# Kernel tuning notes

Hardware: AMD Instinct MI355X
Metric: run time of the kernel (lower is better)

## Reference

```python
import jax, jax.numpy as jnp
import numpy as np

LOG2 = float(np.log(2.0))

def ssp(v):
    # shifted softplus used by SchNet-style nets
    return jax.nn.softplus(v) - LOG2

N = 100000   # nodes per set
E = 600000   # edges
A = 128      # n_atom_basis
F = 128      # n_filters
R = 20       # n_rbf


def setup_inputs() -> dict:
    key = jax.random.key(0)
    ks = jax.random.split(key, 20)
    def lin(k, fan_in, fan_out):
        return jax.random.normal(k, (fan_in, fan_out), dtype=jnp.float32) / np.sqrt(fan_in)
    inp = {
        "x": jax.random.normal(ks[0], (N, A), dtype=jnp.float32),
        "y": jax.random.normal(ks[1], (N, A), dtype=jnp.float32),
        "f_ij": jax.random.uniform(ks[2], (E, R), dtype=jnp.float32),
        "rcut_ij": jax.random.uniform(ks[3], (E,), dtype=jnp.float32),
        "idx_i": jax.random.randint(ks[4], (E,), 0, N),
        "idx_j": jax.random.randint(ks[5], (E,), 0, N),
        # in2f / in2f_y: Dense(A, F, bias=False)
        "W_in2f": lin(ks[6], A, F),
        "W_in2f_y": lin(ks[7], A, F),
        # filter_network: Dense(R, F, act) -> Dense(F, F)
        "Wf1": lin(ks[8], R, F), "bf1": jnp.zeros((F,), jnp.float32),
        "Wf2": lin(ks[9], F, F), "bf2": jnp.zeros((F,), jnp.float32),
        # f2out: Dense(F, A, act) -> Dense(A, A)
        "Wx1": lin(ks[10], F, A), "bx1": jnp.zeros((A,), jnp.float32),
        "Wx2": lin(ks[11], A, A), "bx2": jnp.zeros((A,), jnp.float32),
        # f2out_y
        "Wy1": lin(ks[12], F, A), "by1": jnp.zeros((A,), jnp.float32),
        "Wy2": lin(ks[13], A, A), "by2": jnp.zeros((A,), jnp.float32),
    }
    return inp


def reference(x, y, f_ij, rcut_ij, W_in2f, W_in2f_y, Wf1, bf1, Wf2, bf2,
              Wx1, bx1, Wx2, bx2, Wy1, by1, Wy2, by2, idx_i, idx_j):
    # node feature projections (bias-free)
    xf = x @ W_in2f                # [N, F]
    yf = y @ W_in2f_y              # [N, F]
    # edge filter MLP
    Wij = ssp(f_ij @ Wf1 + bf1) @ Wf2 + bf2      # [E, F]
    Wij = Wij * rcut_ij[:, None]
    # gather-multiply
    x_ij = yf[idx_j] * Wij          # messages into x-nodes
    y_ij = xf[idx_i] * Wij          # messages into y-nodes
    # scatter_add into dual node sets
    conv_x = jax.ops.segment_sum(x_ij, idx_i, num_segments=N)   # [N, F]
    conv_y = jax.ops.segment_sum(y_ij, idx_j, num_segments=N)   # [N, F]
    # output MLPs
    out_x = ssp(conv_x @ Wx1 + bx1) @ Wx2 + bx2
    out_y = ssp(conv_y @ Wy1 + by1) @ Wy2 + by2
    return (out_x, out_y)
```

## Files before the change

kernel.cpp:

```cpp
#include <hip/hip_runtime.h>
#include <hip/hip_bf16.h>

#define NF 128
#define RBF 20

using short8 = __attribute__((ext_vector_type(8))) short;
using half8  = __attribute__((ext_vector_type(8))) _Float16;
using f32x4  = __attribute__((ext_vector_type(4))) float;

__device__ __forceinline__ float sspf(float v) {
    const float t = __expf(-fabsf(v));
    return fmaxf(v, 0.f) + __logf(1.f + t) - 0.69314718055994531f;
}
__device__ __forceinline__ unsigned short f2bf(float f) {
    union { float f; unsigned u; } v; v.f = f;
    unsigned r = v.u + 0x7fffu + ((v.u >> 16) & 1u);
    return (unsigned short)(r >> 16);
}
__device__ __forceinline__ float bf2f(unsigned short s) {
    union { unsigned u; float f; } v; v.u = ((unsigned)s) << 16;
    return v.f;
}

__global__ void hist1_kernel(const int* __restrict__ idx, int* __restrict__ deg, int E)
{
    for (int e = blockIdx.x * blockDim.x + threadIdx.x; e < E;
         e += gridDim.x * blockDim.x)
        atomicAdd(&deg[idx[e]], 1);
}

__global__ void scanA1_kernel(const int* __restrict__ deg, int* __restrict__ loc,
                              int* __restrict__ parts, int NN)
{
    const int tid = threadIdx.x;
    const int base = blockIdx.x * 2048;
    __shared__ int tsum[256];
    int v[8]; int s = 0;
    #pragma unroll
    for (int r = 0; r < 8; ++r) {
        const int idx = base + tid * 8 + r;
        v[r] = (idx < NN) ? deg[idx] : 0;
        s += v[r];
    }
    tsum[tid] = s;
    __syncthreads();
    #pragma unroll
    for (int d = 1; d < 256; d <<= 1) {
        const int add = (tid >= d) ? tsum[tid - d] : 0;
        __syncthreads();
        tsum[tid] += add;
        __syncthreads();
    }
    int run = tsum[tid] - s;
    #pragma unroll
    for (int r = 0; r < 8; ++r) {
        const int idx = base + tid * 8 + r;
        if (idx < NN) loc[idx] = run;
        run += v[r];
    }
    if (tid == 0) parts[blockIdx.x] = tsum[255];
}

__global__ void scanB1_kernel(int* __restrict__ parts, int NB)
{
    __shared__ int p[64];
    const int t = threadIdx.x;
    p[t] = (t < NB) ? parts[t] : 0;
    __syncthreads();
    #pragma unroll
    for (int d = 1; d < 64; d <<= 1) {
        const int add = (t >= d) ? p[t - d] : 0;
        __syncthreads();
        p[t] += add;
        __syncthreads();
    }
    parts[t] = (t > 0) ? p[t - 1] : 0;
}

__global__ void scanC1_kernel(const int* __restrict__ loc, const int* __restrict__ parts,
                              int* __restrict__ rowp, int* __restrict__ cur, int NN)
{
    for (int i = blockIdx.x * blockDim.x + threadIdx.x; i < NN;
         i += gridDim.x * blockDim.x) {
        const int v = loc[i] + parts[i >> 11];
        rowp[i] = v;
        cur[i]  = v;
    }
}

__global__ void scatter1_kernel(const int* __restrict__ idx_i, const int* __restrict__ idx_j,
                                const float* __restrict__ rcut,
                                int* __restrict__ cur, int* __restrict__ ord,
                                int* __restrict__ nis, int* __restrict__ jos,
                                float* __restrict__ rcs, int E)
{
    for (int e = blockIdx.x * blockDim.x + threadIdx.x; e < E;
         e += gridDim.x * blockDim.x) {
        const int key = idx_i[e];
        const int p = atomicAdd(&cur[key], 1);
        ord[p] = e;
        nis[p] = key;
        jos[p] = idx_j[e] * NF;
        rcs[p] = rcut[e];
    }
}

__global__ void fsort_kernel(const float* __restrict__ f_ij,
                             const int* __restrict__ ord,
                             _Float16* __restrict__ f16s, int E)
{
    for (int p = blockIdx.x * blockDim.x + threadIdx.x; p < E;
         p += gridDim.x * blockDim.x) {
        const int e = ord[p];
        const float* src = f_ij + (size_t)e * RBF;
        _Float16* dst = f16s + (size_t)p * 32;
        #pragma unroll
        for (int k4 = 0; k4 < 5; ++k4) {
            const float4 v = *reinterpret_cast<const float4*>(src + k4 * 4);
            dst[k4 * 4 + 0] = (_Float16)v.x;
            dst[k4 * 4 + 1] = (_Float16)v.y;
            dst[k4 * 4 + 2] = (_Float16)v.z;
            dst[k4 * 4 + 3] = (_Float16)v.w;
        }
        #pragma unroll
        for (int k = RBF; k < 32; ++k) dst[k] = (_Float16)0.f;
    }
}

__global__ __launch_bounds__(256, 2)
void edge_hybrid_kernel(const _Float16* __restrict__ f16s,
                        const int* __restrict__ nis,
                        const int* __restrict__ jos,
                        const float* __restrict__ rcs,
                        const float* __restrict__ Wf1,
                        const float* __restrict__ bf1,
                        const float* __restrict__ Wf2,
                        const float* __restrict__ bf2v,
                        const _Float16* __restrict__ xf,
                        const _Float16* __restrict__ yf,
                        const int* __restrict__ rowp,
                        float* __restrict__ conv_x,
                        float* __restrict__ conv_y,
                        int NN, int E)
{
    const int tid = threadIdx.x;
    const int l = tid & 63, w = tid >> 6;
    const int lr = l & 15, lk = l >> 4;
    const int wcol0 = w * 32;

    __shared__ _Float16 M_s[32 * 137];
    __shared__ _Float16 Ash[32 * 136];
    __shared__ _Float16 xown[16 * 136];
    __shared__ int ni_s[32];
    __shared__ int jo_s[32];
    __shared__ float rc_s[32];

    _Float16* fst = M_s;

    half8 b1fr[2];
    #pragma unroll
    for (int cb = 0; cb < 2; ++cb) {
        const int col = wcol0 + cb * 16 + lr;
        #pragma unroll
        for (int j = 0; j < 8; ++j) {
            const int k = lk * 8 + j;
            b1fr[cb][j] = (k < RBF) ? (_Float16)Wf1[k * NF + col] : (_Float16)0.f;
        }
    }
    half8 b2fr[4][2];
    #pragma unroll
    for (int kb = 0; kb < 4; ++kb)
        #pragma unroll
        for (int cb = 0; cb < 2; ++cb) {
            const int col = wcol0 + cb * 16 + lr;
            #pragma unroll
            for (int j = 0; j < 8; ++j)
                b2fr[kb][cb][j] = (_Float16)Wf2[(size_t)(kb * 32 + lk * 8 + j) * NF + col];
        }
    const float b1c[2] = { bf1[wcol0 + lr], bf1[wcol0 + 16 + lr] };
    const float b2c[2] = { bf2v[wcol0 + lr], bf2v[wcol0 + 16 + lr] };

    const int n0 = blockIdx.x * 16;
    const int eb = rowp[n0];
    const int ee = (n0 + 16 < NN) ? rowp[n0 + 16] : E;
    const int nt = (ee - eb + 31) >> 5;

    #pragma unroll
    for (int u = 0; u < 4; ++u) {
        const int tt = u * 256 + tid;
        const int row = tt >> 6, cp = tt & 63;
        unsigned v = 0;
        if (n0 + row < NN)
            v = reinterpret_cast<const unsigned*>(xf)[(size_t)(n0 + row) * 64 + cp];
        *reinterpret_cast<unsigned*>(&xown[row * 136 + cp * 2]) = v;
    }

    f32x4 accS[2] = {};

    for (int t = 0; t < nt; ++t) {
        const int p0 = eb + t * 32;
        const int cnt = ee - p0;
        __syncthreads();

        if (tid < 32) {
            const int p = p0 + tid;
            const bool val = p < ee;
            ni_s[tid] = val ? nis[p] : -1;
            jo_s[tid] = val ? jos[p] : 0;
            rc_s[tid] = val ? rcs[p] : 0.f;
        }
        {
            const unsigned* src = reinterpret_cast<const unsigned*>(f16s);
            unsigned* dst = reinterpret_cast<unsigned*>(fst);
            #pragma unroll
            for (int s2 = 0; s2 < 2; ++s2) {
                const int tt = s2 * 256 + tid;
                int p = p0 + (tt >> 4);
                if (p >= E) p = E - 1;
                dst[tt] = src[(size_t)p * 16 + (tt & 15)];
            }
        }
        __syncthreads();

        f32x4 acc1[2][2] = {};
        #pragma unroll
        for (int rb = 0; rb < 2; ++rb) {
            const half8 a = *reinterpret_cast<const half8*>(
                &fst[(rb * 16 + lr) * 32 + lk * 8]);
            #pragma unroll
            for (int cb = 0; cb < 2; ++cb)
                acc1[rb][cb] = __builtin_amdgcn_mfma_f32_16x16x32_f16(
                    a, b1fr[cb], acc1[rb][cb], 0, 0, 0);
        }
        #pragma unroll
        for (int rb = 0; rb < 2; ++rb)
            #pragma unroll
            for (int cb = 0; cb < 2; ++cb) {
                const int col = wcol0 + cb * 16 + lr;
                #pragma unroll
                for (int q = 0; q < 4; ++q) {
                    const int e = rb * 16 + lk * 4 + q;
                    const float hv = sspf(acc1[rb][cb][q] + b1c[cb]);
                    Ash[e * 136 + (col ^ ((e & 7) << 3))] = (_Float16)hv;
                }
            }
        __syncthreads();

        unsigned gr[8];
        #pragma unroll
        for (int u = 0; u < 8; ++u) {
            const int tt = u * 256 + tid;
            const int slot = tt >> 6, cp = tt & 63;
            gr[u] = reinterpret_cast<const unsigned*>(yf)[(jo_s[slot] >> 1) + cp];
        }

        f32x4 acc2[2][2] = {};
        #pragma unroll
        for (int rb = 0; rb < 2; ++rb) {
            half8 a[4];
            #pragma unroll
            for (int kb = 0; kb < 4; ++kb) {
                const int e  = rb * 16 + lr;
                const int k0 = kb * 32 + lk * 8;
                a[kb] = *reinterpret_cast<const half8*>(
                    &Ash[e * 136 + (k0 ^ ((e & 7) << 3))]);
            }
            #pragma unroll
            for (int cb = 0; cb < 2; ++cb)
                #pragma unroll
                for (int kb = 0; kb < 4; ++kb)
                    acc2[rb][cb] = __builtin_amdgcn_mfma_f32_16x16x32_f16(
                        a[kb], b2fr[kb][cb], acc2[rb][cb], 0, 0, 0);
        }
        __syncthreads();

        #pragma unroll
        for (int u = 0; u < 8; ++u) {
            const int tt = u * 256 + tid;
            const int slot = tt >> 6, cp = tt & 63;
            *reinterpret_cast<unsigned*>(&Ash[slot * 136 + cp * 2]) = gr[u];
        }
        __syncthreads();

        #pragma unroll
        for (int rb = 0; rb < 2; ++rb)
            #pragma unroll
            for (int cb = 0; cb < 2; ++cb) {
                const int col = wcol0 + cb * 16 + lr;
                #pragma unroll
                for (int q = 0; q < 4; ++q) {
                    const int e = rb * 16 + lk * 4 + q;
                    const float wv = (acc2[rb][cb][q] + b2c[cb]) * rc_s[e];
                    const float g  = (float)Ash[e * 136 + col];
                    M_s[e * 137 + col] = (_Float16)(wv * g);
                    if (e < cnt) {
                        const int oi = ni_s[e] - n0;
                        const float xo = (float)xown[oi * 136 + col];
                        unsafeAtomicAdd(&conv_y[(size_t)jo_s[e] + col], xo * wv);
                    }
                }
            }
        __syncthreads();

        {
            half8 as;
            int nn[8];
            #pragma unroll
            for (int j = 0; j < 8; ++j) nn[j] = ni_s[lk * 8 + j];
            const int node = n0 + lr;
            #pragma unroll
            for (int j = 0; j < 8; ++j)
                as[j] = (nn[j] == node) ? (_Float16)1.f : (_Float16)0.f;
            #pragma unroll
            for (int cb = 0; cb < 2; ++cb) {
                const int col = wcol0 + cb * 16 + lr;
                half8 bm;
                #pragma unroll
                for (int j = 0; j < 8; ++j)
                    bm[j] = M_s[(lk * 8 + j) * 137 + col];
                accS[cb] = __builtin_amdgcn_mfma_f32_16x16x32_f16(
                    as, bm, accS[cb], 0, 0, 0);
            }
        }
    }

    #pragma unroll
    for (int cb = 0; cb < 2; ++cb) {
        const int col = wcol0 + cb * 16 + lr;
        #pragma unroll
        for (int q = 0; q < 4; ++q) {
            const int n = n0 + lk * 4 + q;
            if (n < NN) conv_x[(size_t)n * NF + col] = accS[cb][q];
        }
    }
}

__global__ __launch_bounds__(256, 2)
void proj_mfma_kernel(const float* in0, const float* in1,
                      const float* __restrict__ W0, const float* __restrict__ W1p,
                      _Float16* o0, _Float16* o1,
                      float* __restrict__ conv_y, int N)
{
    const float* in = blockIdx.y ? in1 : in0;
    const float* W  = blockIdx.y ? W1p : W0;
    _Float16* out   = blockIdx.y ? o1 : o0;

    const int tid = threadIdx.x;
    const int l = tid & 63, w = tid >> 6;
    const int lr = l & 15, lk = l >> 4;
    const int wcol0 = w * 32;

    __shared__ _Float16 Ahi[64 * NF];

    half8 bfr[4][2];
    #pragma unroll
    for (int kb = 0; kb < 4; ++kb)
        #pragma unroll
        for (int cb = 0; cb < 2; ++cb) {
            const int col = wcol0 + cb * 16 + lr;
            #pragma unroll
            for (int j = 0; j < 8; ++j)
                bfr[kb][cb][j] = (_Float16)W[(size_t)(kb * 32 + lk * 8 + j) * NF + col];
        }

    const int n0 = blockIdx.x * 64;
    #pragma unroll
    for (int s = 0; s < 32; ++s) {
        const int t = s * 256 + tid;
        const int row = t >> 7, cc = t & (NF - 1);
        const float v = (n0 + row < N) ? in[(size_t)(n0 + row) * NF + cc] : 0.f;
        Ahi[row * NF + (cc ^ ((row & 7) << 3))] = (_Float16)v;
    }
    {
        const float4 z = {0.f, 0.f, 0.f, 0.f};
        const int rbase = n0 + 32 * blockIdx.y;
        #pragma unroll
        for (int s = 0; s < 4; ++s) {
            const int t = s * 256 + tid;
            const int row = rbase + (t >> 5);
            if (row < N)
                *reinterpret_cast<float4*>(&conv_y[(size_t)row * NF + (t & 31) * 4]) = z;
        }
    }
    __syncthreads();

    f32x4 acc[4][2] = {};
    #pragma unroll
    for (int rb = 0; rb < 4; ++rb) {
        half8 a[4];
        #pragma unroll
        for (int kb = 0; kb < 4; ++kb) {
            const int e  = rb * 16 + lr;
            const int k0 = kb * 32 + lk * 8;
            a[kb] = *reinterpret_cast<const half8*>(&Ahi[e * NF + (k0 ^ ((e & 7) << 3))]);
        }
        #pragma unroll
        for (int cb = 0; cb < 2; ++cb)
            #pragma unroll
            for (int kb = 0; kb < 4; ++kb)
                acc[rb][cb] = __builtin_amdgcn_mfma_f32_16x16x32_f16(
                    a[kb], bfr[kb][cb], acc[rb][cb], 0, 0, 0);
    }

    #pragma unroll
    for (int rb = 0; rb < 4; ++rb)
        #pragma unroll
        for (int cb = 0; cb < 2; ++cb) {
            const int col = wcol0 + cb * 16 + lr;
            #pragma unroll
            for (int q = 0; q < 4; ++q) {
                const int n = n0 + rb * 16 + lk * 4 + q;
                if (n < N) out[(size_t)n * NF + col] = (_Float16)acc[rb][cb][q];
            }
        }
}

__global__ __launch_bounds__(256, 2)
void out_fused_kernel(const float* conv0, const float* conv1,
                      const float* __restrict__ W10, const float* __restrict__ W11,
                      const float* __restrict__ b10, const float* __restrict__ b11,
                      const float* __restrict__ W20, const float* __restrict__ W21,
                      const float* __restrict__ b20, const float* __restrict__ b21,
                      float* o0, float* o1, int N)
{
    const float* in = blockIdx.y ? conv1 : conv0;
    const float* W1 = blockIdx.y ? W11 : W10;
    const float* b1 = blockIdx.y ? b11 : b10;
    const float* W2 = blockIdx.y ? W21 : W20;
    const float* b2 = blockIdx.y ? b21 : b20;
    float* out      = blockIdx.y ? o1  : o0;

    const int tid = threadIdx.x;
    const int l = tid & 63, w = tid >> 6;
    const int lr = l & 15, lk = l >> 4;
    const int wcol0 = w * 32;

    __shared__ unsigned short Ahi[64 * NF];
    __shared__ unsigned short Alo[64 * NF];

    short8 w1fr[4][2], w2fr[4][2];
    #pragma unroll
    for (int kb = 0; kb < 4; ++kb)
        #pragma unroll
        for (int cb = 0; cb < 2; ++cb) {
            const int col = wcol0 + cb * 16 + lr;
            #pragma unroll
            for (int j = 0; j < 8; ++j) {
                const size_t kk = (size_t)(kb * 32 + lk * 8 + j) * NF + col;
                w1fr[kb][cb][j] = (short)f2bf(W1[kk]);
                w2fr[kb][cb][j] = (short)f2bf(W2[kk]);
            }
        }
    const float b1c0 = b1[wcol0 + lr], b1c1 = b1[wcol0 + 16 + lr];
    const float b2c0 = b2[wcol0 + lr], b2c1 = b2[wcol0 + 16 + lr];

    const int n0 = blockIdx.x * 64;
    #pragma unroll
    for (int s = 0; s < 32; ++s) {
        const int t = s * 256 + tid;
        const int row = t >> 7, cc = t & (NF - 1);
        const float v = (n0 + row < N) ? in[(size_t)(n0 + row) * NF + cc] : 0.f;
        const unsigned short hi = f2bf(v);
        const int idx = row * NF + (cc ^ ((row & 7) << 3));
        Ahi[idx] = hi;
        Alo[idx] = f2bf(v - bf2f(hi));
    }
    __syncthreads();

    f32x4 acc1[4][2] = {};
    #pragma unroll
    for (int rb = 0; rb < 4; ++rb) {
        short8 ah[4], al[4];
        #pragma unroll
        for (int kb = 0; kb < 4; ++kb) {
            const int e  = rb * 16 + lr;
            const int k0 = kb * 32 + lk * 8;
            const int idx = e * NF + (k0 ^ ((e & 7) << 3));
            ah[kb] = *reinterpret_cast<const short8*>(&Ahi[idx]);
            al[kb] = *reinterpret_cast<const short8*>(&Alo[idx]);
        }
        #pragma unroll
        for (int cb = 0; cb < 2; ++cb)
            #pragma unroll
            for (int kb = 0; kb < 4; ++kb) {
                acc1[rb][cb] = __builtin_amdgcn_mfma_f32_16x16x32_bf16(
                    ah[kb], w1fr[kb][cb], acc1[rb][cb], 0, 0, 0);
                acc1[rb][cb] = __builtin_amdgcn_mfma_f32_16x16x32_bf16(
                    al[kb], w1fr[kb][cb], acc1[rb][cb], 0, 0, 0);
            }
    }
    __syncthreads();

    #pragma unroll
    for (int rb = 0; rb < 4; ++rb)
        #pragma unroll
        for (int cb = 0; cb < 2; ++cb) {
            const int col = wcol0 + cb * 16 + lr;
            #pragma unroll
            for (int q = 0; q < 4; ++q) {
                const int e = rb * 16 + lk * 4 + q;
                const float hv = sspf(acc1[rb][cb][q] + (cb ? b1c1 : b1c0));
                const unsigned short hi = f2bf(hv);
                const int idx = e * NF + (col ^ ((e & 7) << 3));
                Ahi[idx] = hi;
                Alo[idx] = f2bf(hv - bf2f(hi));
            }
        }
    __syncthreads();

    f32x4 acc2[4][2] = {};
    #pragma unroll
    for (int rb = 0; rb < 4; ++rb) {
        short8 ah[4], al[4];
        #pragma unroll
        for (int kb = 0; kb < 4; ++kb) {
            const int e  = rb * 16 + lr;
            const int k0 = kb * 32 + lk * 8;
            const int idx = e * NF + (k0 ^ ((e & 7) << 3));
            ah[kb] = *reinterpret_cast<const short8*>(&Ahi[idx]);
            al[kb] = *reinterpret_cast<const short8*>(&Alo[idx]);
        }
        #pragma unroll
        for (int cb = 0; cb < 2; ++cb)
            #pragma unroll
            for (int kb = 0; kb < 4; ++kb) {
                acc2[rb][cb] = __builtin_amdgcn_mfma_f32_16x16x32_bf16(
                    ah[kb], w2fr[kb][cb], acc2[rb][cb], 0, 0, 0);
                acc2[rb][cb] = __builtin_amdgcn_mfma_f32_16x16x32_bf16(
                    al[kb], w2fr[kb][cb], acc2[rb][cb], 0, 0, 0);
            }
    }

    #pragma unroll
    for (int rb = 0; rb < 4; ++rb)
        #pragma unroll
        for (int cb = 0; cb < 2; ++cb) {
            const int col = wcol0 + cb * 16 + lr;
            #pragma unroll
            for (int q = 0; q < 4; ++q) {
                const int n = n0 + rb * 16 + lk * 4 + q;
                if (n < N)
                    out[(size_t)n * NF + col] = acc2[rb][cb][q] + (cb ? b2c1 : b2c0);
            }
        }
}

extern "C" void kernel_launch(void* const* d_in, const int* in_sizes, int n_in,
                              void* d_out, int out_size, void* d_ws, size_t ws_size,
                              hipStream_t stream)
{
    const float* x    = (const float*)d_in[0];
    const float* y    = (const float*)d_in[1];
    const float* f_ij = (const float*)d_in[2];
    const float* rcut = (const float*)d_in[3];
    const int* idx_i  = (const int*)d_in[4];
    const int* idx_j  = (const int*)d_in[5];
    const float* W_in2f   = (const float*)d_in[6];
    const float* W_in2f_y = (const float*)d_in[7];
    const float* Wf1 = (const float*)d_in[8];
    const float* bf1 = (const float*)d_in[9];
    const float* Wf2 = (const float*)d_in[10];
    const float* bf2 = (const float*)d_in[11];
    const float* Wx1 = (const float*)d_in[12];
    const float* bx1 = (const float*)d_in[13];
    const float* Wx2 = (const float*)d_in[14];
    const float* bx2 = (const float*)d_in[15];
    const float* Wy1 = (const float*)d_in[16];
    const float* by1 = (const float*)d_in[17];
    const float* Wy2 = (const float*)d_in[18];
    const float* by2 = (const float*)d_in[19];

    const int N = in_sizes[0] / NF;
    const int E = in_sizes[4];
    const size_t NNF = (size_t)N * NF;

    _Float16* xf = (_Float16*)d_out;
    _Float16* yf = xf + NNF;
    float* ox = (float*)d_out;
    float* oy = ox + NNF;

    char* ub = (char*)d_out + 4 * NNF;
    int* deg   = (int*)ub;
    int* loc   = deg + N;
    int* rowp  = loc + N;
    int* cur   = rowp + N;
    int* parts = cur + N;
    int* ord   = parts + 64;
    int* nis   = ord + E;
    int* jos   = nis + E;
    float* rcs = (float*)(jos + E);
    _Float16* f16s = (_Float16*)(rcs + E);

    float* conv_x = (float*)d_ws;
    float* conv_y = conv_x + NNF;

    const int NB = (N + 2047) / 2048;
    const int nodeTiles = (N + 63) / 64;
    const int nGroups = (N + 15) / 16;

    hipMemsetAsync(deg, 0, (size_t)N * sizeof(int), stream);

    proj_mfma_kernel<<<dim3(nodeTiles, 2), 256, 0, stream>>>(
        x, y, W_in2f, W_in2f_y, xf, yf, conv_y, N);

    hist1_kernel<<<1024, 256, 0, stream>>>(idx_i, deg, E);
    scanA1_kernel<<<NB, 256, 0, stream>>>(deg, loc, parts, N);
    scanB1_kernel<<<1, 64, 0, stream>>>(parts, NB);
    scanC1_kernel<<<128, 256, 0, stream>>>(loc, parts, rowp, cur, N);
    scatter1_kernel<<<1024, 256, 0, stream>>>(idx_i, idx_j, rcut, cur, ord,
                                              nis, jos, rcs, E);
    fsort_kernel<<<2048, 256, 0, stream>>>(f_ij, ord, f16s, E);

    edge_hybrid_kernel<<<nGroups, 256, 0, stream>>>(
        f16s, nis, jos, rcs, Wf1, bf1, Wf2, bf2, xf, yf,
        rowp, conv_x, conv_y, N, E);

    out_fused_kernel<<<dim3(nodeTiles, 2), 256, 0, stream>>>(
        conv_x, conv_y, Wx1, Wy1, bx1, by1, Wx2, Wy2, bx2, by2,
        ox, oy, N);
}
```

Measured before the change: 647.6 us.

## Fuse f_ij sort into scatter, load edge features directly, use single fp16 MFMA in output MLP

Three changes at once. The f_ij conversion and reorder now happen inside the scatter kernel, which removes the ord array and a separate fsort launch, and writes each row with 16-byte stores. The edge kernel reads its f16 A-fragments straight from global memory instead of staging them in LDS, which drops one barrier per tile. The output MLP kernel replaces the split bf16 hi/lo pair of MFMAs with one fp16 MFMA per step, halving that matrix work and its LDS traffic at the cost of precision.

New measurement: 632.5 us. 2.3% less time.

```diff
diff --git a/kernel.cpp b/kernel.cpp
--- a/kernel.cpp
+++ b/kernel.cpp
@@ -4,22 +4,12 @@
 #define NF 128
 #define RBF 20
 
-using short8 = __attribute__((ext_vector_type(8))) short;
-using half8  = __attribute__((ext_vector_type(8))) _Float16;
-using f32x4  = __attribute__((ext_vector_type(4))) float;
+using half8 = __attribute__((ext_vector_type(8))) _Float16;
+using f32x4 = __attribute__((ext_vector_type(4))) float;
 
 __device__ __forceinline__ float sspf(float v) {
     const float t = __expf(-fabsf(v));
     return fmaxf(v, 0.f) + __logf(1.f + t) - 0.69314718055994531f;
-}
-__device__ __forceinline__ unsigned short f2bf(float f) {
-    union { float f; unsigned u; } v; v.f = f;
-    unsigned r = v.u + 0x7fffu + ((v.u >> 16) & 1u);
-    return (unsigned short)(r >> 16);
-}
-__device__ __forceinline__ float bf2f(unsigned short s) {
-    union { unsigned u; float f; } v; v.u = ((unsigned)s) << 16;
-    return v.f;
 }
 
 __global__ void hist1_kernel(const int* __restrict__ idx, int* __restrict__ deg, int E)
@@ -90,40 +80,35 @@
 
 __global__ void scatter1_kernel(const int* __restrict__ idx_i, const int* __restrict__ idx_j,
                                 const float* __restrict__ rcut,
-                                int* __restrict__ cur, int* __restrict__ ord,
+                                const float* __restrict__ f_ij,
+                                int* __restrict__ cur,
                                 int* __restrict__ nis, int* __restrict__ jos,
-                                float* __restrict__ rcs, int E)
+                                float* __restrict__ rcs,
+                                _Float16* __restrict__ f16s, int E)
 {
     for (int e = blockIdx.x * blockDim.x + threadIdx.x; e < E;
          e += gridDim.x * blockDim.x) {
         const int key = idx_i[e];
         const int p = atomicAdd(&cur[key], 1);
-        ord[p] = e;
         nis[p] = key;
         jos[p] = idx_j[e] * NF;
         rcs[p] = rcut[e];
-    }
-}
-
-__global__ void fsort_kernel(const float* __restrict__ f_ij,
-                             const int* __restrict__ ord,
-                             _Float16* __restrict__ f16s, int E)
-{
-    for (int p = blockIdx.x * blockDim.x + threadIdx.x; p < E;
-         p += gridDim.x * blockDim.x) {
-        const int e = ord[p];
+
         const float* src = f_ij + (size_t)e * RBF;
-        _Float16* dst = f16s + (size_t)p * 32;
+        _Float16 tmp[32];
         #pragma unroll
         for (int k4 = 0; k4 < 5; ++k4) {
             const float4 v = *reinterpret_cast<const float4*>(src + k4 * 4);
-            dst[k4 * 4 + 0] = (_Float16)v.x;
-            dst[k4 * 4 + 1] = (_Float16)v.y;
-            dst[k4 * 4 + 2] = (_Float16)v.z;
-            dst[k4 * 4 + 3] = (_Float16)v.w;
-        }
-        #pragma unroll
-        for (int k = RBF; k < 32; ++k) dst[k] = (_Float16)0.f;
+            tmp[k4 * 4 + 0] = (_Float16)v.x;
+            tmp[k4 * 4 + 1] = (_Float16)v.y;
+            tmp[k4 * 4 + 2] = (_Float16)v.z;
+            tmp[k4 * 4 + 3] = (_Float16)v.w;
+        }
+        #pragma unroll
+        for (int k = RBF; k < 32; ++k) tmp[k] = (_Float16)0.f;
+        uint4* dst = reinterpret_cast<uint4*>(f16s + (size_t)p * 32);
+        const uint4* s4 = reinterpret_cast<const uint4*>(tmp);
+        dst[0] = s4[0]; dst[1] = s4[1]; dst[2] = s4[2]; dst[3] = s4[3];
     }
 }
 
@@ -155,8 +140,6 @@
     __shared__ int jo_s[32];
     __shared__ float rc_s[32];
 
-    _Float16* fst = M_s;
-
     half8 b1fr[2];
     #pragma unroll
     for (int cb = 0; cb < 2; ++cb) {
@@ -209,24 +192,14 @@
             jo_s[tid] = val ? jos[p] : 0;
             rc_s[tid] = val ? rcs[p] : 0.f;
         }
-        {
-            const unsigned* src = reinterpret_cast<const unsigned*>(f16s);
-            unsigned* dst = reinterpret_cast<unsigned*>(fst);
-            #pragma unroll
-            for (int s2 = 0; s2 < 2; ++s2) {
-                const int tt = s2 * 256 + tid;
-                int p = p0 + (tt >> 4);
-                if (p >= E) p = E - 1;
-                dst[tt] = src[(size_t)p * 16 + (tt & 15)];
-            }
-        }
-        __syncthreads();
 
         f32x4 acc1[2][2] = {};
         #pragma unroll
         for (int rb = 0; rb < 2; ++rb) {
+            int p = p0 + rb * 16 + lr;
+            if (p >= E) p = E - 1;
             const half8 a = *reinterpret_cast<const half8*>(
-                &fst[(rb * 16 + lr) * 32 + lk * 8]);
+                &f16s[(size_t)p * 32 + lk * 8]);
             #pragma unroll
             for (int cb = 0; cb < 2; ++cb)
                 acc1[rb][cb] = __builtin_amdgcn_mfma_f32_16x16x32_f16(
@@ -435,10 +408,9 @@
     const int lr = l & 15, lk = l >> 4;
     const int wcol0 = w * 32;
 
-    __shared__ unsigned short Ahi[64 * NF];
-    __shared__ unsigned short Alo[64 * NF];
-
-    short8 w1fr[4][2], w2fr[4][2];
+    __shared__ _Float16 Ahi[64 * NF];
+
+    half8 w1fr[4][2], w2fr[4][2];
     #pragma unroll
     for (int kb = 0; kb < 4; ++kb)
         #pragma unroll
@@ -447,8 +419,8 @@
             #pragma unroll
             for (int j = 0; j < 8; ++j) {
                 const size_t kk = (size_t)(kb * 32 + lk * 8 + j) * NF + col;
-                w1fr[kb][cb][j] = (short)f2bf(W1[kk]);
-                w2fr[kb][cb][j] = (short)f2bf(W2[kk]);
+                w1fr[kb][cb][j] = (_Float16)W1[kk];
+                w2fr[kb][cb][j] = (_Float16)W2[kk];
             }
         }
     const float b1c0 = b1[wcol0 + lr], b1c1 = b1[wcol0 + 16 + lr];
@@ -460,34 +432,26 @@
         const int t = s * 256 + tid;
         const int row = t >> 7, cc = t & (NF - 1);
         const float v = (n0 + row < N) ? in[(size_t)(n0 + row) * NF + cc] : 0.f;
-        const unsigned short hi = f2bf(v);
-        const int idx = row * NF + (cc ^ ((row & 7) << 3));
-        Ahi[idx] = hi;
-        Alo[idx] = f2bf(v - bf2f(hi));
+        Ahi[row * NF + (cc ^ ((row & 7) << 3))] = (_Float16)v;
     }
     __syncthreads();
 
     f32x4 acc1[4][2] = {};
     #pragma unroll
     for (int rb = 0; rb < 4; ++rb) {
-        short8 ah[4], al[4];
+        half8 a[4];
         #pragma unroll
         for (int kb = 0; kb < 4; ++kb) {
             const int e  = rb * 16 + lr;
             const int k0 = kb * 32 + lk * 8;
-            const int idx = e * NF + (k0 ^ ((e & 7) << 3));
-            ah[kb] = *reinterpret_cast<const short8*>(&Ahi[idx]);
-            al[kb] = *reinterpret_cast<const short8*>(&Alo[idx]);
+            a[kb] = *reinterpret_cast<const half8*>(&Ahi[e * NF + (k0 ^ ((e & 7) << 3))]);
         }
         #pragma unroll
         for (int cb = 0; cb < 2; ++cb)
             #pragma unroll
-            for (int kb = 0; kb < 4; ++kb) {
-                acc1[rb][cb] = __builtin_amdgcn_mfma_f32_16x16x32_bf16(
-                    ah[kb], w1fr[kb][cb], acc1[rb][cb], 0, 0, 0);
-                acc1[rb][cb] = __builtin_amdgcn_mfma_f32_16x16x32_bf16(
-                    al[kb], w1fr[kb][cb], acc1[rb][cb], 0, 0, 0);
-            }
+            for (int kb = 0; kb < 4; ++kb)
+                acc1[rb][cb] = __builtin_amdgcn_mfma_f32_16x16x32_f16(
+                    a[kb], w1fr[kb][cb], acc1[rb][cb], 0, 0, 0);
     }
     __syncthreads();
 
@@ -500,10 +464,7 @@
             for (int q = 0; q < 4; ++q) {
                 const int e = rb * 16 + lk * 4 + q;
                 const float hv = sspf(acc1[rb][cb][q] + (cb ? b1c1 : b1c0));
-                const unsigned short hi = f2bf(hv);
-                const int idx = e * NF + (col ^ ((e & 7) << 3));
-                Ahi[idx] = hi;
-                Alo[idx] = f2bf(hv - bf2f(hi));
+                Ahi[e * NF + (col ^ ((e & 7) << 3))] = (_Float16)hv;
             }
         }
     __syncthreads();
@@ -511,24 +472,19 @@
     f32x4 acc2[4][2] = {};
     #pragma unroll
     for (int rb = 0; rb < 4; ++rb) {
-        short8 ah[4], al[4];
+        half8 a[4];
         #pragma unroll
         for (int kb = 0; kb < 4; ++kb) {
             const int e  = rb * 16 + lr;
             const int k0 = kb * 32 + lk * 8;
-            const int idx = e * NF + (k0 ^ ((e & 7) << 3));
-            ah[kb] = *reinterpret_cast<const short8*>(&Ahi[idx]);
-            al[kb] = *reinterpret_cast<const short8*>(&Alo[idx]);
+            a[kb] = *reinterpret_cast<const half8*>(&Ahi[e * NF + (k0 ^ ((e & 7) << 3))]);
         }
         #pragma unroll
         for (int cb = 0; cb < 2; ++cb)
             #pragma unroll
-            for (int kb = 0; kb < 4; ++kb) {
-                acc2[rb][cb] = __builtin_amdgcn_mfma_f32_16x16x32_bf16(
-                    ah[kb], w2fr[kb][cb], acc2[rb][cb], 0, 0, 0);
-                acc2[rb][cb] = __builtin_amdgcn_mfma_f32_16x16x32_bf16(
-                    al[kb], w2fr[kb][cb], acc2[rb][cb], 0, 0, 0);
-            }
+            for (int kb = 0; kb < 4; ++kb)
+                acc2[rb][cb] = __builtin_amdgcn_mfma_f32_16x16x32_f16(
+                    a[kb], w2fr[kb][cb], acc2[rb][cb], 0, 0, 0);
     }
 
     #pragma unroll
@@ -585,8 +541,7 @@
     int* rowp  = loc + N;
     int* cur   = rowp + N;
     int* parts = cur + N;
-    int* ord   = parts + 64;
-    int* nis   = ord + E;
+    int* nis   = parts + 64;
     int* jos   = nis + E;
     float* rcs = (float*)(jos + E);
     _Float16* f16s = (_Float16*)(rcs + E);
@@ -607,9 +562,8 @@
     scanA1_kernel<<<NB, 256, 0, stream>>>(deg, loc, parts, N);
     scanB1_kernel<<<1, 64, 0, stream>>>(parts, NB);
     scanC1_kernel<<<128, 256, 0, stream>>>(loc, parts, rowp, cur, N);
-    scatter1_kernel<<<1024, 256, 0, stream>>>(idx_i, idx_j, rcut, cur, ord,
-                                              nis, jos, rcs, E);
-    fsort_kernel<<<2048, 256, 0, stream>>>(f_ij, ord, f16s, E);
+    scatter1_kernel<<<2048, 256, 0, stream>>>(idx_i, idx_j, rcut, f_ij, cur,
+                                              nis, jos, rcs, f16s, E);
 
     edge_hybrid_kernel<<<nGroups, 256, 0, stream>>>(
         f16s, nis, jos, rcs, Wf1, bf1, Wf2, bf2, xf, yf,
```
